# Kernel tuning notes

Measured on AMD Instinct MI355X. Metric: run time of the kernel, lower is better.

## Reference

```python
import jax, jax.numpy as jnp
import numpy as np

B, L, D = 8, 256, 256  # batch, max sentence length, channel_in == channel_out


def setup_inputs() -> dict:
    key = jax.random.key(0)
    k1, k2, k3, k4, k5, k6 = jax.random.split(key, 6)
    queries = jax.random.normal(k1, (B, L, D), dtype=jnp.float32)
    wordlens = jax.random.randint(k2, (B,), 1, L, dtype=jnp.int32)
    syntactic_dep = jax.random.randint(k3, (B, L, L), 0, 2, dtype=jnp.int32)
    # w_wc[0]: Linear(2D -> D, no bias); split its weight into the h_i and h_j halves.
    s1 = 1.0 / np.sqrt(2 * D)
    Wa = jax.random.normal(k4, (D, D), dtype=jnp.float32) * s1
    Wb = jax.random.normal(jax.random.fold_in(k4, 1), (D, D), dtype=jnp.float32) * s1
    # w_wc[3]: Linear(D -> 1, no bias)
    w2 = jax.random.normal(k5, (D,), dtype=jnp.float32) * (1.0 / np.sqrt(D))
    # wd: Linear(D -> D, no bias)
    Wd = jax.random.normal(k6, (D, D), dtype=jnp.float32) * (1.0 / np.sqrt(D))
    return {"queries": queries, "wordlens": wordlens, "syntactic_dep": syntactic_dep,
            "Wa": Wa, "Wb": Wb, "w2": w2, "Wd": Wd}


def reference(queries, wordlens, syntactic_dep, Wa, Wb, w2, Wd):
    # queries: [B, L, D]; syntactic_dep: [B, L, L] (nonzero => edge i->j)
    mask = syntactic_dep > 0
    # Edge score t_ij = w2 . relu(Wa h_i + Wb h_j)  (dropout is identity at eval)
    A = jnp.einsum('bid,cd->bic', queries, Wa)   # [B, L, C]
    Bm = jnp.einsum('bjd,cd->bjc', queries, Wb)  # [B, L, C]
    pre = jax.nn.relu(A[:, :, None, :] + Bm[:, None, :, :])  # [B, L, L, C]
    t = jnp.einsum('bijc,c->bij', pre, w2)       # [B, L, L]
    # T initialized to -100 everywhere, edge positions get t (exactly as original)
    T = jnp.where(mask, t, jnp.float32(-100.0))
    beta = jax.nn.softmax(T, axis=-1)            # softmax over j (dim=1 of [L, L])
    w = beta * mask.astype(beta.dtype)           # zero out non-edges after softmax
    hj = jnp.einsum('bjd,cd->bjc', queries, Wd)  # wd(h_j), [B, L, C]
    agg = jnp.einsum('bij,bjc->bic', w, hj)      # weighted neighbor sum
    output = jax.nn.relu(queries + agg)
    # skip=False, so no extra residual add
    return (output, wordlens, syntactic_dep)
```

## Files before the change

kernel.cpp:

```cpp
#include <hip/hip_runtime.h>

#define NB 8
#define LL 256
#define DD 256

typedef __attribute__((ext_vector_type(8))) short short8v;
typedef __attribute__((ext_vector_type(4))) float f32x4;

__device__ __forceinline__ uint f2bf2(float lo, float hi) {
  uint a = __float_as_uint(lo), b = __float_as_uint(hi);
  uint ra = (a + 0x7FFFu + ((a >> 16) & 1u)) >> 16;
  uint rb = (b + 0x7FFFu + ((b >> 16) & 1u)) & 0xFFFF0000u;
  return ra | rb;
}

__global__ __launch_bounds__(256) void gemm3_mfma(
    const float* __restrict__ Q, const float* __restrict__ Wa,
    const float* __restrict__ Wb, const float* __restrict__ Wd,
    const int* __restrict__ wl, const int* __restrict__ sdep,
    float* __restrict__ A, float* __restrict__ Bm, float* __restrict__ Hj,
    float* __restrict__ tail) {
  const int mt = blockIdx.x, nt = blockIdx.y, z = blockIdx.z;
  const int bid = mt + 32 * (nt + 4 * z);
  const float* __restrict__ W = (z == 0) ? Wa : (z == 1) ? Wb : Wd;
  float* __restrict__ Out = (z == 0) ? A : (z == 1) ? Bm : Hj;

  __shared__ __align__(16) ushort Qs[64][32];
  __shared__ __align__(16) ushort Ws[64][32];

  const int tid = threadIdx.x;
  const int m0 = mt * 64, n0 = nt * 64;
  const int srow = tid >> 2, skc = (tid & 3) * 8;
  const int w = tid >> 6, lane = tid & 63;
  const int wm = w >> 1, wn = w & 1;
  const int fr = lane & 15, fk = (lane >> 4) * 8;

  f32x4 acc[2][2] = {};
  for (int k0 = 0; k0 < DD; k0 += 32) {
    {
      const float* src = &Q[(size_t)(m0 + srow) * DD + k0 + skc];
      float4 q0 = *(const float4*)src;
      float4 q1 = *(const float4*)(src + 4);
      uint4 pk = make_uint4(f2bf2(q0.x, q0.y), f2bf2(q0.z, q0.w),
                            f2bf2(q1.x, q1.y), f2bf2(q1.z, q1.w));
      *(uint4*)&Qs[srow][skc] = pk;
      const float* ws_ = &W[(size_t)(n0 + srow) * DD + k0 + skc];
      float4 w0 = *(const float4*)ws_;
      float4 w1 = *(const float4*)(ws_ + 4);
      uint4 pw = make_uint4(f2bf2(w0.x, w0.y), f2bf2(w0.z, w0.w),
                            f2bf2(w1.x, w1.y), f2bf2(w1.z, w1.w));
      *(uint4*)&Ws[srow][skc] = pw;
    }
    __syncthreads();
    short8v a0 = *(const short8v*)&Qs[wm * 32 + fr][fk];
    short8v a1 = *(const short8v*)&Qs[wm * 32 + 16 + fr][fk];
    short8v b0 = *(const short8v*)&Ws[wn * 32 + fr][fk];
    short8v b1 = *(const short8v*)&Ws[wn * 32 + 16 + fr][fk];
    acc[0][0] = __builtin_amdgcn_mfma_f32_16x16x32_bf16(a0, b0, acc[0][0], 0, 0, 0);
    acc[0][1] = __builtin_amdgcn_mfma_f32_16x16x32_bf16(a0, b1, acc[0][1], 0, 0, 0);
    acc[1][0] = __builtin_amdgcn_mfma_f32_16x16x32_bf16(a1, b0, acc[1][0], 0, 0, 0);
    acc[1][1] = __builtin_amdgcn_mfma_f32_16x16x32_bf16(a1, b1, acc[1][1], 0, 0, 0);
    __syncthreads();
  }

  const int rbase = m0 + wm * 32 + (lane >> 4) * 4;
  const int cbase = n0 + wn * 32 + fr;
#pragma unroll
  for (int i = 0; i < 2; ++i)
#pragma unroll
    for (int j = 0; j < 2; ++j)
#pragma unroll
      for (int r = 0; r < 4; ++r)
        Out[(size_t)(rbase + i * 16 + r) * DD + cbase + j * 16] = acc[i][j][r];

  for (int t = bid * 256 + tid; t < 131072; t += 384 * 256) {
    int4 s = *(const int4*)&sdep[(size_t)t * 4];
    float4 f;
    f.x = (float)s.x; f.y = (float)s.y; f.z = (float)s.z; f.w = (float)s.w;
    *(float4*)&tail[8 + (size_t)t * 4] = f;
  }
  if (bid == 0 && tid < 8) tail[tid] = (float)wl[tid];
}

__global__ __launch_bounds__(512, 2) void fused_kernel(
    const float* __restrict__ Q, const int* __restrict__ sdep,
    const float* __restrict__ w2, const float* __restrict__ A,
    const float* __restrict__ Bm, const float* __restrict__ Hj,
    float* __restrict__ out) {
  const int bid = blockIdx.x;
  const int b = bid & 7, it = bid >> 3;
  const int i0 = it * 8;
  const int tid = threadIdx.x;
  const int w = tid >> 6, l = tid & 63;
  const int j0 = w * 32;

  __shared__ float Ts[8][260];
  __shared__ float Red[8][4][256];

  {
    const int jp = l >> 4;
    const int cg = l & 15;
    float a[8][16], wv[16];
    const float* Ab = A + ((size_t)(b * LL + i0)) * DD + cg * 16;
#pragma unroll
    for (int r = 0; r < 8; ++r)
#pragma unroll
      for (int ch = 0; ch < 4; ++ch)
        *(float4*)&a[r][ch * 4] = *(const float4*)&Ab[(size_t)r * DD + ch * 4];
#pragma unroll
    for (int ch = 0; ch < 4; ++ch)
      *(float4*)&wv[ch * 4] = *(const float4*)&w2[cg * 16 + ch * 4];

    const float* Bb = Bm + ((size_t)(b * LL + j0 + jp)) * DD + cg * 16;
#pragma unroll 2
    for (int s = 0; s < 8; ++s) {
      float bv[16];
#pragma unroll
      for (int ch = 0; ch < 4; ++ch)
        *(float4*)&bv[ch * 4] =
            *(const float4*)&Bb[(size_t)(s * 4) * DD + ch * 4];
      float p0 = 0.f, p1 = 0.f, p2 = 0.f, p3 = 0.f;
      float p4 = 0.f, p5 = 0.f, p6 = 0.f, p7 = 0.f;
#pragma unroll
      for (int u = 0; u < 16; ++u) {
        float bb = bv[u], ww = wv[u];
        p0 = fmaf(ww, fmaxf(a[0][u] + bb, 0.f), p0);
        p1 = fmaf(ww, fmaxf(a[1][u] + bb, 0.f), p1);
        p2 = fmaf(ww, fmaxf(a[2][u] + bb, 0.f), p2);
        p3 = fmaf(ww, fmaxf(a[3][u] + bb, 0.f), p3);
        p4 = fmaf(ww, fmaxf(a[4][u] + bb, 0.f), p4);
        p5 = fmaf(ww, fmaxf(a[5][u] + bb, 0.f), p5);
        p6 = fmaf(ww, fmaxf(a[6][u] + bb, 0.f), p6);
        p7 = fmaf(ww, fmaxf(a[7][u] + bb, 0.f), p7);
      }
#pragma unroll
      for (int m = 1; m <= 8; m <<= 1) {
        p0 += __shfl_xor(p0, m); p1 += __shfl_xor(p1, m);
        p2 += __shfl_xor(p2, m); p3 += __shfl_xor(p3, m);
        p4 += __shfl_xor(p4, m); p5 += __shfl_xor(p5, m);
        p6 += __shfl_xor(p6, m); p7 += __shfl_xor(p7, m);
      }
      float pv = p0;
      pv = (cg == 1) ? p1 : pv; pv = (cg == 2) ? p2 : pv;
      pv = (cg == 3) ? p3 : pv; pv = (cg == 4) ? p4 : pv;
      pv = (cg == 5) ? p5 : pv; pv = (cg == 6) ? p6 : pv;
      pv = (cg == 7) ? p7 : pv;
      if (cg < 8) Ts[cg][j0 + s * 4 + jp] = pv;
    }
  }
  __syncthreads();

  {
    const int* sr = sdep + ((size_t)(b * LL + i0 + w)) * LL;
    float v[4];
    float m = -3.0e38f;
#pragma unroll
    for (int k = 0; k < 4; ++k) {
      int j = l + 64 * k;
      bool e = sr[j] > 0;
      v[k] = e ? Ts[w][j] : -3.0e38f;
      m = fmaxf(m, v[k]);
    }
#pragma unroll
    for (int off = 32; off >= 1; off >>= 1) m = fmaxf(m, __shfl_xor(m, off));
    float s = 0.f;
#pragma unroll
    for (int k = 0; k < 4; ++k) {
      float e = (v[k] > -1.0e30f) ? __expf(v[k] - m) : 0.f;
      v[k] = e;
      s += e;
    }
#pragma unroll
    for (int off = 32; off >= 1; off >>= 1) s += __shfl_xor(s, off);
    float inv = (s > 0.f) ? 1.0f / s : 0.f;
    __syncthreads();
#pragma unroll
    for (int k = 0; k < 4; ++k) Ts[w][l + 64 * k] = v[k] * inv;
  }
  __syncthreads();

  const float* Hb = Hj + ((size_t)(b * LL + j0)) * DD + l * 4;
#pragma unroll
  for (int g = 0; g < 2; ++g) {
    {
      float acc[4][4] = {};
#pragma unroll 2
      for (int j4 = 0; j4 < 8; ++j4) {
        float tw0[4], tw1[4], tw2[4], tw3[4];
        *(float4*)tw0 = *(const float4*)&Ts[g * 4 + 0][j0 + j4 * 4];
        *(float4*)tw1 = *(const float4*)&Ts[g * 4 + 1][j0 + j4 * 4];
        *(float4*)tw2 = *(const float4*)&Ts[g * 4 + 2][j0 + j4 * 4];
        *(float4*)tw3 = *(const float4*)&Ts[g * 4 + 3][j0 + j4 * 4];
#pragma unroll
        for (int u = 0; u < 4; ++u) {
          float4 h = *(const float4*)&Hb[(size_t)(j4 * 4 + u) * DD];
          acc[0][0] = fmaf(tw0[u], h.x, acc[0][0]);
          acc[0][1] = fmaf(tw0[u], h.y, acc[0][1]);
          acc[0][2] = fmaf(tw0[u], h.z, acc[0][2]);
          acc[0][3] = fmaf(tw0[u], h.w, acc[0][3]);
          acc[1][0] = fmaf(tw1[u], h.x, acc[1][0]);
          acc[1][1] = fmaf(tw1[u], h.y, acc[1][1]);
          acc[1][2] = fmaf(tw1[u], h.z, acc[1][2]);
          acc[1][3] = fmaf(tw1[u], h.w, acc[1][3]);
          acc[2][0] = fmaf(tw2[u], h.x, acc[2][0]);
          acc[2][1] = fmaf(tw2[u], h.y, acc[2][1]);
          acc[2][2] = fmaf(tw2[u], h.z, acc[2][2]);
          acc[2][3] = fmaf(tw2[u], h.w, acc[2][3]);
          acc[3][0] = fmaf(tw3[u], h.x, acc[3][0]);
          acc[3][1] = fmaf(tw3[u], h.y, acc[3][1]);
          acc[3][2] = fmaf(tw3[u], h.z, acc[3][2]);
          acc[3][3] = fmaf(tw3[u], h.w, acc[3][3]);
        }
      }
#pragma unroll
      for (int r = 0; r < 4; ++r)
        *(float4*)&Red[w][r][l * 4] = *(float4*)acc[r];
    }
    __syncthreads();
    if (tid < 256) {
      const int r = tid >> 6, q = tid & 63;
      float4 s0 = *(const float4*)&Red[0][r][q * 4];
      float4 s1 = *(const float4*)&Red[1][r][q * 4];
      float4 s2 = *(const float4*)&Red[2][r][q * 4];
      float4 s3 = *(const float4*)&Red[3][r][q * 4];
      float4 s4 = *(const float4*)&Red[4][r][q * 4];
      float4 s5 = *(const float4*)&Red[5][r][q * 4];
      float4 s6 = *(const float4*)&Red[6][r][q * 4];
      float4 s7 = *(const float4*)&Red[7][r][q * 4];
      size_t off = ((size_t)(b * LL + i0 + g * 4 + r)) * DD + q * 4;
      float4 qv = *(const float4*)&Q[off];
      float4 o;
      o.x = fmaxf(qv.x + ((s0.x + s1.x) + (s2.x + s3.x)) +
                          ((s4.x + s5.x) + (s6.x + s7.x)), 0.f);
      o.y = fmaxf(qv.y + ((s0.y + s1.y) + (s2.y + s3.y)) +
                          ((s4.y + s5.y) + (s6.y + s7.y)), 0.f);
      o.z = fmaxf(qv.z + ((s0.z + s1.z) + (s2.z + s3.z)) +
                          ((s4.z + s5.z) + (s6.z + s7.z)), 0.f);
      o.w = fmaxf(qv.w + ((s0.w + s1.w) + (s2.w + s3.w)) +
                          ((s4.w + s5.w) + (s6.w + s7.w)), 0.f);
      *(float4*)&out[off] = o;
    }
    __syncthreads();
  }
}

extern "C" void kernel_launch(void* const* d_in, const int* in_sizes, int n_in,
                              void* d_out, int out_size, void* d_ws, size_t ws_size,
                              hipStream_t stream) {
  const float* Q    = (const float*)d_in[0];
  const int*   wl   = (const int*)d_in[1];
  const int*   sdep = (const int*)d_in[2];
  const float* Wa   = (const float*)d_in[3];
  const float* Wb   = (const float*)d_in[4];
  const float* w2   = (const float*)d_in[5];
  const float* Wd   = (const float*)d_in[6];
  float* out = (float*)d_out;
  float* ws  = (float*)d_ws;

  float* A  = ws;
  float* Bm = ws + 524288;
  float* Hj = ws + 1048576;
  float* tail = out + (size_t)NB * LL * DD;

  gemm3_mfma<<<dim3(32, 4, 3), 256, 0, stream>>>(Q, Wa, Wb, Wd, wl, sdep,
                                                 A, Bm, Hj, tail);
  fused_kernel<<<256, 512, 0, stream>>>(Q, sdep, w2, A, Bm, Hj, out);
}
```

Before: 102.9 us.

## Pack edge-score math into float2 ops and halve GEMM N-tile

The pairwise edge-score loop in the fused kernel now uses two-wide float vectors with elementwise max/fma builtins, so the compiler can emit packed FP32 instructions (v_pk_add/v_pk_fma) and halve the VALU instruction count for the relu-dot. Each partial sum is now split across two lanes that are added at the end, which changes the summation order slightly. Separately, the projection GEMM uses 64x32 output tiles, giving twice as many blocks (768), with a min-blocks launch bound of 3. The sdep-to-float tail copy becomes one element per thread because the grid now covers the whole range.

```diff
diff --git a/kernel.cpp b/kernel.cpp
--- a/kernel.cpp
+++ b/kernel.cpp
@@ -6,6 +6,13 @@
 
 typedef __attribute__((ext_vector_type(8))) short short8v;
 typedef __attribute__((ext_vector_type(4))) float f32x4;
+typedef __attribute__((ext_vector_type(2))) float f32x2;
+
+#if defined(__has_builtin)
+#if __has_builtin(__builtin_elementwise_fma) && __has_builtin(__builtin_elementwise_max)
+#define USE_PK 1
+#endif
+#endif
 
 __device__ __forceinline__ uint f2bf2(float lo, float hi) {
   uint a = __float_as_uint(lo), b = __float_as_uint(hi);
@@ -14,28 +21,28 @@
   return ra | rb;
 }
 
-__global__ __launch_bounds__(256) void gemm3_mfma(
+__global__ __launch_bounds__(256, 3) void gemm3_mfma(
     const float* __restrict__ Q, const float* __restrict__ Wa,
     const float* __restrict__ Wb, const float* __restrict__ Wd,
     const int* __restrict__ wl, const int* __restrict__ sdep,
     float* __restrict__ A, float* __restrict__ Bm, float* __restrict__ Hj,
     float* __restrict__ tail) {
   const int mt = blockIdx.x, nt = blockIdx.y, z = blockIdx.z;
-  const int bid = mt + 32 * (nt + 4 * z);
+  const int bid = mt + 32 * (nt + 8 * z);
   const float* __restrict__ W = (z == 0) ? Wa : (z == 1) ? Wb : Wd;
   float* __restrict__ Out = (z == 0) ? A : (z == 1) ? Bm : Hj;
 
   __shared__ __align__(16) ushort Qs[64][32];
-  __shared__ __align__(16) ushort Ws[64][32];
+  __shared__ __align__(16) ushort Ws[32][32];
 
   const int tid = threadIdx.x;
-  const int m0 = mt * 64, n0 = nt * 64;
+  const int m0 = mt * 64, n0 = nt * 32;
   const int srow = tid >> 2, skc = (tid & 3) * 8;
   const int w = tid >> 6, lane = tid & 63;
   const int wm = w >> 1, wn = w & 1;
   const int fr = lane & 15, fk = (lane >> 4) * 8;
 
-  f32x4 acc[2][2] = {};
+  f32x4 acc[2] = {};
   for (int k0 = 0; k0 < DD; k0 += 32) {
     {
       const float* src = &Q[(size_t)(m0 + srow) * DD + k0 + skc];
@@ -44,6 +51,8 @@
       uint4 pk = make_uint4(f2bf2(q0.x, q0.y), f2bf2(q0.z, q0.w),
                             f2bf2(q1.x, q1.y), f2bf2(q1.z, q1.w));
       *(uint4*)&Qs[srow][skc] = pk;
+    }
+    if (tid < 128) {
       const float* ws_ = &W[(size_t)(n0 + srow) * DD + k0 + skc];
       float4 w0 = *(const float4*)ws_;
       float4 w1 = *(const float4*)(ws_ + 4);
@@ -54,30 +63,28 @@
     __syncthreads();
     short8v a0 = *(const short8v*)&Qs[wm * 32 + fr][fk];
     short8v a1 = *(const short8v*)&Qs[wm * 32 + 16 + fr][fk];
-    short8v b0 = *(const short8v*)&Ws[wn * 32 + fr][fk];
-    short8v b1 = *(const short8v*)&Ws[wn * 32 + 16 + fr][fk];
-    acc[0][0] = __builtin_amdgcn_mfma_f32_16x16x32_bf16(a0, b0, acc[0][0], 0, 0, 0);
-    acc[0][1] = __builtin_amdgcn_mfma_f32_16x16x32_bf16(a0, b1, acc[0][1], 0, 0, 0);
-    acc[1][0] = __builtin_amdgcn_mfma_f32_16x16x32_bf16(a1, b0, acc[1][0], 0, 0, 0);
-    acc[1][1] = __builtin_amdgcn_mfma_f32_16x16x32_bf16(a1, b1, acc[1][1], 0, 0, 0);
+    short8v b0 = *(const short8v*)&Ws[wn * 16 + fr][fk];
+    acc[0] = __builtin_amdgcn_mfma_f32_16x16x32_bf16(a0, b0, acc[0], 0, 0, 0);
+    acc[1] = __builtin_amdgcn_mfma_f32_16x16x32_bf16(a1, b0, acc[1], 0, 0, 0);
     __syncthreads();
   }
 
   const int rbase = m0 + wm * 32 + (lane >> 4) * 4;
-  const int cbase = n0 + wn * 32 + fr;
+  const int cbase = n0 + wn * 16 + fr;
 #pragma unroll
   for (int i = 0; i < 2; ++i)
 #pragma unroll
-    for (int j = 0; j < 2; ++j)
-#pragma unroll
-      for (int r = 0; r < 4; ++r)
-        Out[(size_t)(rbase + i * 16 + r) * DD + cbase + j * 16] = acc[i][j][r];
-
-  for (int t = bid * 256 + tid; t < 131072; t += 384 * 256) {
-    int4 s = *(const int4*)&sdep[(size_t)t * 4];
-    float4 f;
-    f.x = (float)s.x; f.y = (float)s.y; f.z = (float)s.z; f.w = (float)s.w;
-    *(float4*)&tail[8 + (size_t)t * 4] = f;
+    for (int r = 0; r < 4; ++r)
+      Out[(size_t)(rbase + i * 16 + r) * DD + cbase] = acc[i][r];
+
+  {
+    int t = bid * 256 + tid;
+    if (t < 131072) {
+      int4 s = *(const int4*)&sdep[(size_t)t * 4];
+      float4 f;
+      f.x = (float)s.x; f.y = (float)s.y; f.z = (float)s.z; f.w = (float)s.w;
+      *(float4*)&tail[8 + (size_t)t * 4] = f;
+    }
   }
   if (bid == 0 && tid < 8) tail[tid] = (float)wl[tid];
 }
@@ -100,48 +107,63 @@
   {
     const int jp = l >> 4;
     const int cg = l & 15;
-    float a[8][16], wv[16];
+    f32x2 a2[8][8], wv2[8];
     const float* Ab = A + ((size_t)(b * LL + i0)) * DD + cg * 16;
 #pragma unroll
     for (int r = 0; r < 8; ++r)
 #pragma unroll
-      for (int ch = 0; ch < 4; ++ch)
-        *(float4*)&a[r][ch * 4] = *(const float4*)&Ab[(size_t)r * DD + ch * 4];
-#pragma unroll
-    for (int ch = 0; ch < 4; ++ch)
-      *(float4*)&wv[ch * 4] = *(const float4*)&w2[cg * 16 + ch * 4];
+      for (int ch = 0; ch < 4; ++ch) {
+        float4 t = *(const float4*)&Ab[(size_t)r * DD + ch * 4];
+        a2[r][ch * 2] = (f32x2){t.x, t.y};
+        a2[r][ch * 2 + 1] = (f32x2){t.z, t.w};
+      }
+#pragma unroll
+    for (int ch = 0; ch < 4; ++ch) {
+      float4 t = *(const float4*)&w2[cg * 16 + ch * 4];
+      wv2[ch * 2] = (f32x2){t.x, t.y};
+      wv2[ch * 2 + 1] = (f32x2){t.z, t.w};
+    }
 
     const float* Bb = Bm + ((size_t)(b * LL + j0 + jp)) * DD + cg * 16;
 #pragma unroll 2
     for (int s = 0; s < 8; ++s) {
-      float bv[16];
-#pragma unroll
-      for (int ch = 0; ch < 4; ++ch)
-        *(float4*)&bv[ch * 4] =
-            *(const float4*)&Bb[(size_t)(s * 4) * DD + ch * 4];
-      float p0 = 0.f, p1 = 0.f, p2 = 0.f, p3 = 0.f;
-      float p4 = 0.f, p5 = 0.f, p6 = 0.f, p7 = 0.f;
-#pragma unroll
-      for (int u = 0; u < 16; ++u) {
-        float bb = bv[u], ww = wv[u];
-        p0 = fmaf(ww, fmaxf(a[0][u] + bb, 0.f), p0);
-        p1 = fmaf(ww, fmaxf(a[1][u] + bb, 0.f), p1);
-        p2 = fmaf(ww, fmaxf(a[2][u] + bb, 0.f), p2);
-        p3 = fmaf(ww, fmaxf(a[3][u] + bb, 0.f), p3);
-        p4 = fmaf(ww, fmaxf(a[4][u] + bb, 0.f), p4);
-        p5 = fmaf(ww, fmaxf(a[5][u] + bb, 0.f), p5);
-        p6 = fmaf(ww, fmaxf(a[6][u] + bb, 0.f), p6);
-        p7 = fmaf(ww, fmaxf(a[7][u] + bb, 0.f), p7);
-      }
+      f32x2 bv2[8];
+#pragma unroll
+      for (int ch = 0; ch < 4; ++ch) {
+        float4 t = *(const float4*)&Bb[(size_t)(s * 4) * DD + ch * 4];
+        bv2[ch * 2] = (f32x2){t.x, t.y};
+        bv2[ch * 2 + 1] = (f32x2){t.z, t.w};
+      }
+      f32x2 p2[8] = {};
+#pragma unroll
+      for (int u = 0; u < 8; ++u) {
+        f32x2 bb = bv2[u], ww = wv2[u];
+#pragma unroll
+        for (int r = 0; r < 8; ++r) {
+#ifdef USE_PK
+          f32x2 sm = __builtin_elementwise_max(a2[r][u] + bb, (f32x2){0.f, 0.f});
+          p2[r] = __builtin_elementwise_fma(ww, sm, p2[r]);
+#else
+          f32x2 t0 = a2[r][u] + bb;
+          f32x2 sm = {fmaxf(t0.x, 0.f), fmaxf(t0.y, 0.f)};
+          p2[r].x = fmaf(ww.x, sm.x, p2[r].x);
+          p2[r].y = fmaf(ww.y, sm.y, p2[r].y);
+#endif
+        }
+      }
+      float p0 = p2[0].x + p2[0].y, p1 = p2[1].x + p2[1].y;
+      float p2s = p2[2].x + p2[2].y, p3 = p2[3].x + p2[3].y;
+      float p4 = p2[4].x + p2[4].y, p5 = p2[5].x + p2[5].y;
+      float p6 = p2[6].x + p2[6].y, p7 = p2[7].x + p2[7].y;
 #pragma unroll
       for (int m = 1; m <= 8; m <<= 1) {
         p0 += __shfl_xor(p0, m); p1 += __shfl_xor(p1, m);
-        p2 += __shfl_xor(p2, m); p3 += __shfl_xor(p3, m);
+        p2s += __shfl_xor(p2s, m); p3 += __shfl_xor(p3, m);
         p4 += __shfl_xor(p4, m); p5 += __shfl_xor(p5, m);
         p6 += __shfl_xor(p6, m); p7 += __shfl_xor(p7, m);
       }
       float pv = p0;
-      pv = (cg == 1) ? p1 : pv; pv = (cg == 2) ? p2 : pv;
+      pv = (cg == 1) ? p1 : pv; pv = (cg == 2) ? p2s : pv;
       pv = (cg == 3) ? p3 : pv; pv = (cg == 4) ? p4 : pv;
       pv = (cg == 5) ? p5 : pv; pv = (cg == 6) ? p6 : pv;
       pv = (cg == 7) ? p7 : pv;
@@ -262,7 +284,7 @@
   float* Hj = ws + 1048576;
   float* tail = out + (size_t)NB * LL * DD;
 
-  gemm3_mfma<<<dim3(32, 4, 3), 256, 0, stream>>>(Q, Wa, Wb, Wd, wl, sdep,
+  gemm3_mfma<<<dim3(32, 8, 3), 256, 0, stream>>>(Q, Wa, Wb, Wd, wl, sdep,
                                                  A, Bm, Hj, tail);
   fused_kernel<<<256, 512, 0, stream>>>(Q, sdep, w2, A, Bm, Hj, out);
 }
```

Measured after the change: 100.7 us. 2.2% less time.
